# Kernel optimization log

Hardware: AMD Instinct MI355X
Metric: run time of the kernel (lower is better)

Reference implementation:

```python
import jax, jax.numpy as jnp
import numpy as np

B, N, E, DIN, DOUT = 4, 10000, 320000, 128, 128
EPS = 1e-5


def setup_inputs() -> dict:
    key = jax.random.key(0)
    ks = jax.random.split(key, 10)
    x = jax.random.normal(ks[0], (B, N, DIN), dtype=jnp.float32)
    edge_index = jax.random.randint(ks[1], (2, E), 0, N, dtype=jnp.int64)
    norm = jax.random.uniform(ks[2], (E, 1), dtype=jnp.float32)
    W_w = jax.random.normal(ks[3], (DOUT, DIN), dtype=jnp.float32) / np.sqrt(DIN)
    W_b = jax.random.normal(ks[4], (DOUT,), dtype=jnp.float32) * 0.01
    bn_gamma = jnp.ones((N,), dtype=jnp.float32)
    bn_beta = jnp.zeros((N,), dtype=jnp.float32)
    bn_mean = jax.random.normal(ks[5], (N,), dtype=jnp.float32) * 0.01
    bn_var = jax.random.uniform(ks[6], (N,), dtype=jnp.float32, minval=0.5, maxval=1.5)
    return {"x": x, "edge_index": edge_index, "norm": norm, "W_w": W_w,
            "W_b": W_b, "bn_gamma": bn_gamma, "bn_beta": bn_beta,
            "bn_mean": bn_mean, "bn_var": bn_var}


def reference(x, edge_index, norm, W_w, W_b, bn_gamma, bn_beta, bn_mean, bn_var):
    # Dropout is identity in eval mode.
    h = jnp.einsum('bnf,of->bno', x, W_w) + W_b            # [B, N, DOUT]
    # BatchNorm1d over channel dim = node dim (eval mode, running stats)
    inv = jax.lax.rsqrt(bn_var + EPS)
    h = (h - bn_mean[None, :, None]) * (inv * bn_gamma)[None, :, None] + bn_beta[None, :, None]
    h = jax.nn.gelu(h, approximate=False)                  # torch GELU default = exact erf
    # gather -> scale -> scatter-add message passing
    msgs = h[:, edge_index[1], :] * norm                   # [B, E, DOUT]
    out = jnp.zeros_like(h).at[:, edge_index[0], :].add(msgs)
    return out
```

## Files before the change

kernel.cpp:

```cpp
#include <hip/hip_runtime.h>
#include <math.h>

#define DIN 128
#define DOUT 128
#define EPS 1e-5f
#define CAP 128

typedef unsigned short ushort_t;
typedef __bf16 bf16x8 __attribute__((ext_vector_type(8)));
typedef float f32x16 __attribute__((ext_vector_type(16)));

__device__ __forceinline__ unsigned int f2bf_u(float f) {
    union { float f; unsigned int i; } v; v.f = f;
    unsigned int x = v.i;
    unsigned int r = x + 0x7fffu + ((x >> 16) & 1u);
    return r >> 16;
}
__device__ __forceinline__ ushort_t f2bf(float f) { return (ushort_t)f2bf_u(f); }

__global__ __launch_bounds__(256) void prep_kernel(
    const float* __restrict__ W, uint4* __restrict__ wb,
    int* __restrict__ counts, int N)
{
    int t = blockIdx.x * blockDim.x + threadIdx.x;
    if (t < 2048) {
        int ct = t >> 9, kc = (t >> 6) & 7, l = t & 63;
        int o = ct * 32 + (l & 31);
        int f = kc * 16 + ((l >> 5) << 3);
        const float4* src = (const float4*)(W + o * 128 + f);
        float4 v0 = src[0], v1 = src[1];
        uint4 pk;
        pk.x = f2bf_u(v0.x) | (f2bf_u(v0.y) << 16);
        pk.y = f2bf_u(v0.z) | (f2bf_u(v0.w) << 16);
        pk.z = f2bf_u(v1.x) | (f2bf_u(v1.y) << 16);
        pk.w = f2bf_u(v1.z) | (f2bf_u(v1.w) << 16);
        wb[t] = pk;
    }
    for (int i = t; i < N; i += gridDim.x * blockDim.x) counts[i] = 0;
}

__global__ __launch_bounds__(256, 4) void gemm_bn_gelu_fill(
    const float* __restrict__ x, const uint4* __restrict__ wb,
    const float* __restrict__ bias, const float* __restrict__ gamma,
    const float* __restrict__ beta, const float* __restrict__ mean,
    const float* __restrict__ var, ushort_t* __restrict__ hb,
    const int* __restrict__ ei, const float* __restrict__ norm,
    int* __restrict__ counts, unsigned int* __restrict__ csr,
    int N, int E)
{
    __shared__ ushort_t XH[8192];
    __shared__ float sm_mu[16], sm_sc[16], sm_bt[16];

    const int tid = threadIdx.x;
    const int n0 = blockIdx.x * 16;
    const int w = tid >> 6;
    const int lane = tid & 63;

    bf16x8 bfr[8];
#pragma unroll
    for (int kc = 0; kc < 8; ++kc)
        bfr[kc] = *(const bf16x8*)(wb + (w * 512 + kc * 64 + lane));

    {
        const int gid = blockIdx.x * blockDim.x + tid;
        const int stride = gridDim.x * blockDim.x;
        for (int e = gid; e < E; e += 2 * stride) {
            int ep = e + stride;
            int has2 = ep < E;
            int dst0 = ei[e];
            int src0 = ei[E + e];
            float nm0 = norm[e];
            int dst1 = 0, src1 = 0;
            float nm1 = 0.f;
            if (has2) { dst1 = ei[ep]; src1 = ei[E + ep]; nm1 = norm[ep]; }
            int slot0 = atomicAdd(&counts[dst0], 1);
            if (slot0 < CAP)
                csr[(size_t)dst0 * CAP + slot0] =
                    ((unsigned int)src0 << 16) | f2bf_u(nm0);
            if (has2) {
                int slot1 = atomicAdd(&counts[dst1], 1);
                if (slot1 < CAP)
                    csr[(size_t)dst1 * CAP + slot1] =
                        ((unsigned int)src1 << 16) | f2bf_u(nm1);
            }
        }
    }

    if (tid < 16) {
        int n = n0 + tid;
        sm_mu[tid] = mean[n];
        sm_sc[tid] = rsqrtf(var[n] + EPS) * gamma[n];
        sm_bt[tid] = beta[n];
    }

#pragma unroll
    for (int it = 0; it < 4; ++it) {
        int tup = tid + it * 256;
        int rt = tup >> 9, kc = (tup >> 6) & 7, l = tup & 63;
        int r = rt * 32 + (l & 31);
        int b = r >> 4, i = r & 15;
        size_t grow = (size_t)b * N + n0 + i;
        int f = kc * 16 + ((l >> 5) << 3);
        const float4* src = (const float4*)(x + grow * 128 + f);
        float4 v0 = src[0], v1 = src[1];
        uint4 pk;
        pk.x = f2bf_u(v0.x) | (f2bf_u(v0.y) << 16);
        pk.y = f2bf_u(v0.z) | (f2bf_u(v0.w) << 16);
        pk.z = f2bf_u(v1.x) | (f2bf_u(v1.y) << 16);
        pk.w = f2bf_u(v1.z) | (f2bf_u(v1.w) << 16);
        *(uint4*)&XH[tup * 8] = pk;
    }
    __syncthreads();

    f32x16 acc0 = {};
    f32x16 acc1 = {};
#pragma unroll
    for (int kc = 0; kc < 8; ++kc) {
        bf16x8 a0 = *(const bf16x8*)&XH[(kc * 64 + lane) * 8];
        bf16x8 a1 = *(const bf16x8*)&XH[(512 * 8) + (kc * 64 + lane) * 8];
        acc0 = __builtin_amdgcn_mfma_f32_32x32x16_bf16(a0, bfr[kc], acc0, 0, 0, 0);
        acc1 = __builtin_amdgcn_mfma_f32_32x32x16_bf16(a1, bfr[kc], acc1, 0, 0, 0);
    }
    __syncthreads();

    const int col = w * 32 + (lane & 31);
    const float bias_c = bias[col];
    const int hi4 = (lane >> 5) * 4;
#pragma unroll
    for (int reg = 0; reg < 8; ++reg) {
        int i0 = (reg & 3) + 8 * (reg >> 2) + hi4;
        float mu = sm_mu[i0], sc = sm_sc[i0], bt = sm_bt[i0];
        float vals[4] = { acc0[reg], acc0[reg + 8], acc1[reg], acc1[reg + 8] };
        ushort4 pk;
        {
            float v = vals[0] + bias_c; v = (v - mu) * sc + bt;
            pk.x = f2bf(0.5f * v * (1.0f + erff(v * 0.70710678118654752f)));
        }
        {
            float v = vals[1] + bias_c; v = (v - mu) * sc + bt;
            pk.y = f2bf(0.5f * v * (1.0f + erff(v * 0.70710678118654752f)));
        }
        {
            float v = vals[2] + bias_c; v = (v - mu) * sc + bt;
            pk.z = f2bf(0.5f * v * (1.0f + erff(v * 0.70710678118654752f)));
        }
        {
            float v = vals[3] + bias_c; v = (v - mu) * sc + bt;
            pk.w = f2bf(0.5f * v * (1.0f + erff(v * 0.70710678118654752f)));
        }
        *(ushort4*)&XH[((i0 << 7) + col) << 2] = pk;
    }
    __syncthreads();

    {
        const float4* s = (const float4*)XH;
        float4* d = (float4*)(hb + (size_t)n0 * 512);
#pragma unroll
        for (int i = tid; i < 1024; i += 256) d[i] = s[i];
    }
}

__device__ __forceinline__ void fma8(float* acc, int4 h, float wgt) {
    union { unsigned int i; float f; } t;
    unsigned int u;
    u = (unsigned int)h.x;
    t.i = u << 16;          acc[0] = fmaf(t.f, wgt, acc[0]);
    t.i = u & 0xffff0000u;  acc[1] = fmaf(t.f, wgt, acc[1]);
    u = (unsigned int)h.y;
    t.i = u << 16;          acc[2] = fmaf(t.f, wgt, acc[2]);
    t.i = u & 0xffff0000u;  acc[3] = fmaf(t.f, wgt, acc[3]);
    u = (unsigned int)h.z;
    t.i = u << 16;          acc[4] = fmaf(t.f, wgt, acc[4]);
    t.i = u & 0xffff0000u;  acc[5] = fmaf(t.f, wgt, acc[5]);
    u = (unsigned int)h.w;
    t.i = u << 16;          acc[6] = fmaf(t.f, wgt, acc[6]);
    t.i = u & 0xffff0000u;  acc[7] = fmaf(t.f, wgt, acc[7]);
}

__global__ __launch_bounds__(256) void gather_kernel(
    const ushort_t* __restrict__ hb, const int* __restrict__ counts,
    const unsigned int* __restrict__ csr, float* __restrict__ out, int N)
{
    const int w = threadIdx.x >> 6;
    const int lane = threadIdx.x & 63;
    const int n = blockIdx.x * 4 + w;
    if (n >= N) return;

    int cnt = counts[n];
    if (cnt > CAP) cnt = CAP;
    const unsigned int* bucket = csr + (size_t)n * CAP;

    float acc[8] = {};
    for (int base = 0; base < cnt; base += 64) {
        int lim = cnt - base; if (lim > 64) lim = 64;
        unsigned int meta = bucket[base + lane];
        int j = 0;
        for (; j + 8 <= lim; j += 8) {
            unsigned int m0 = (unsigned int)__builtin_amdgcn_readlane((int)meta, j);
            unsigned int m1 = (unsigned int)__builtin_amdgcn_readlane((int)meta, j + 1);
            unsigned int m2 = (unsigned int)__builtin_amdgcn_readlane((int)meta, j + 2);
            unsigned int m3 = (unsigned int)__builtin_amdgcn_readlane((int)meta, j + 3);
            unsigned int m4 = (unsigned int)__builtin_amdgcn_readlane((int)meta, j + 4);
            unsigned int m5 = (unsigned int)__builtin_amdgcn_readlane((int)meta, j + 5);
            unsigned int m6 = (unsigned int)__builtin_amdgcn_readlane((int)meta, j + 6);
            unsigned int m7 = (unsigned int)__builtin_amdgcn_readlane((int)meta, j + 7);
            int4 h0 = *(const int4*)(hb + (size_t)(m0 >> 16) * 512 + lane * 8);
            int4 h1 = *(const int4*)(hb + (size_t)(m1 >> 16) * 512 + lane * 8);
            int4 h2 = *(const int4*)(hb + (size_t)(m2 >> 16) * 512 + lane * 8);
            int4 h3 = *(const int4*)(hb + (size_t)(m3 >> 16) * 512 + lane * 8);
            int4 h4 = *(const int4*)(hb + (size_t)(m4 >> 16) * 512 + lane * 8);
            int4 h5 = *(const int4*)(hb + (size_t)(m5 >> 16) * 512 + lane * 8);
            int4 h6 = *(const int4*)(hb + (size_t)(m6 >> 16) * 512 + lane * 8);
            int4 h7 = *(const int4*)(hb + (size_t)(m7 >> 16) * 512 + lane * 8);
            union { unsigned int i; float f; } wv;
            wv.i = m0 << 16; fma8(acc, h0, wv.f);
            wv.i = m1 << 16; fma8(acc, h1, wv.f);
            wv.i = m2 << 16; fma8(acc, h2, wv.f);
            wv.i = m3 << 16; fma8(acc, h3, wv.f);
            wv.i = m4 << 16; fma8(acc, h4, wv.f);
            wv.i = m5 << 16; fma8(acc, h5, wv.f);
            wv.i = m6 << 16; fma8(acc, h6, wv.f);
            wv.i = m7 << 16; fma8(acc, h7, wv.f);
        }
        for (; j < lim; ++j) {
            unsigned int m = (unsigned int)__builtin_amdgcn_readlane((int)meta, j);
            int4 hv = *(const int4*)(hb + (size_t)(m >> 16) * 512 + lane * 8);
            union { unsigned int i; float f; } wv;
            wv.i = m << 16;
            fma8(acc, hv, wv.f);
        }
    }

    const size_t bstride = (size_t)N * DOUT;
    float* op = out + (size_t)n * DOUT + lane * 2;
#pragma unroll
    for (int b = 0; b < 4; ++b) {
        float2 v; v.x = acc[b]; v.y = acc[4 + b];
        *(float2*)(op + b * bstride) = v;
    }
}

extern "C" void kernel_launch(void* const* d_in, const int* in_sizes, int n_in,
                              void* d_out, int out_size, void* d_ws, size_t ws_size,
                              hipStream_t stream)
{
    const float* x     = (const float*)d_in[0];
    const int*   ei    = (const int*)d_in[1];
    const float* norm  = (const float*)d_in[2];
    const float* W_w   = (const float*)d_in[3];
    const float* W_b   = (const float*)d_in[4];
    const float* gamma = (const float*)d_in[5];
    const float* beta  = (const float*)d_in[6];
    const float* mean  = (const float*)d_in[7];
    const float* var   = (const float*)d_in[8];
    float* out = (float*)d_out;

    const int N = in_sizes[5];
    const int E = in_sizes[2];

    ushort_t* hb      = (ushort_t*)d_ws;
    uint4* wb         = (uint4*)(hb + (size_t)N * 512);
    int* counts       = (int*)(wb + 2048);
    unsigned int* csr = (unsigned int*)(counts + N);

    int prep_blocks = (N + 255) / 256;
    prep_kernel<<<prep_blocks, 256, 0, stream>>>(W_w, wb, counts, N);

    int gemm_blocks = N / 16;
    gemm_bn_gelu_fill<<<gemm_blocks, 256, 0, stream>>>(
        x, wb, W_b, gamma, beta, mean, var, hb, ei, norm, counts, csr, N, E);

    gather_kernel<<<(N + 3) / 4, 256, 0, stream>>>(hb, counts, csr, out, N);
}
```

Measured before the change: 152.1 us.

## Bucket CSR edges per destination by source chunk for gather locality

The per-destination edge bucket is split into sub-buckets keyed by the source-node chunk (2048 nodes), each holding up to 32 entries. The gather then walks the chunks in order, so all waves touch roughly the same region of the bf16 activation table at the same time, which should improve L2 hit rates. In exchange it adds more counters to zero, extra per-chunk loop overhead, and padded 8-wide iterations that read row 0 with zero weight. A per-chunk cap of 32 can drop edges if a chunk holds more than 32 in-edges for one node, where the old cap was 128 per node.

```diff
diff --git a/kernel.cpp b/kernel.cpp
--- a/kernel.cpp
+++ b/kernel.cpp
@@ -4,7 +4,8 @@
 #define DIN 128
 #define DOUT 128
 #define EPS 1e-5f
-#define CAP 128
+#define CHUNK_SHIFT 11
+#define CAPC 32
 
 typedef unsigned short ushort_t;
 typedef __bf16 bf16x8 __attribute__((ext_vector_type(8)));
@@ -20,7 +21,7 @@
 
 __global__ __launch_bounds__(256) void prep_kernel(
     const float* __restrict__ W, uint4* __restrict__ wb,
-    int* __restrict__ counts, int N)
+    int* __restrict__ counts, int total_counts)
 {
     int t = blockIdx.x * blockDim.x + threadIdx.x;
     if (t < 2048) {
@@ -36,7 +37,7 @@
         pk.w = f2bf_u(v1.z) | (f2bf_u(v1.w) << 16);
         wb[t] = pk;
     }
-    for (int i = t; i < N; i += gridDim.x * blockDim.x) counts[i] = 0;
+    for (int i = t; i < total_counts; i += gridDim.x * blockDim.x) counts[i] = 0;
 }
 
 __global__ __launch_bounds__(256, 4) void gemm_bn_gelu_fill(
@@ -46,7 +47,7 @@
     const float* __restrict__ var, ushort_t* __restrict__ hb,
     const int* __restrict__ ei, const float* __restrict__ norm,
     int* __restrict__ counts, unsigned int* __restrict__ csr,
-    int N, int E)
+    int N, int E, int nc)
 {
     __shared__ ushort_t XH[8192];
     __shared__ float sm_mu[16], sm_sc[16], sm_bt[16];
@@ -73,14 +74,16 @@
             int dst1 = 0, src1 = 0;
             float nm1 = 0.f;
             if (has2) { dst1 = ei[ep]; src1 = ei[E + ep]; nm1 = norm[ep]; }
-            int slot0 = atomicAdd(&counts[dst0], 1);
-            if (slot0 < CAP)
-                csr[(size_t)dst0 * CAP + slot0] =
+            int b0 = dst0 * nc + (src0 >> CHUNK_SHIFT);
+            int slot0 = atomicAdd(&counts[b0], 1);
+            if (slot0 < CAPC)
+                csr[((size_t)b0 << 5) + slot0] =
                     ((unsigned int)src0 << 16) | f2bf_u(nm0);
             if (has2) {
-                int slot1 = atomicAdd(&counts[dst1], 1);
-                if (slot1 < CAP)
-                    csr[(size_t)dst1 * CAP + slot1] =
+                int b1 = dst1 * nc + (src1 >> CHUNK_SHIFT);
+                int slot1 = atomicAdd(&counts[b1], 1);
+                if (slot1 < CAPC)
+                    csr[((size_t)b1 << 5) + slot1] =
                         ((unsigned int)src1 << 16) | f2bf_u(nm1);
             }
         }
@@ -179,55 +182,48 @@
 
 __global__ __launch_bounds__(256) void gather_kernel(
     const ushort_t* __restrict__ hb, const int* __restrict__ counts,
-    const unsigned int* __restrict__ csr, float* __restrict__ out, int N)
+    const unsigned int* __restrict__ csr, float* __restrict__ out,
+    int N, int nc)
 {
     const int w = threadIdx.x >> 6;
     const int lane = threadIdx.x & 63;
     const int n = blockIdx.x * 4 + w;
     if (n >= N) return;
 
-    int cnt = counts[n];
-    if (cnt > CAP) cnt = CAP;
-    const unsigned int* bucket = csr + (size_t)n * CAP;
-
     float acc[8] = {};
-    for (int base = 0; base < cnt; base += 64) {
-        int lim = cnt - base; if (lim > 64) lim = 64;
-        unsigned int meta = bucket[base + lane];
-        int j = 0;
-        for (; j + 8 <= lim; j += 8) {
-            unsigned int m0 = (unsigned int)__builtin_amdgcn_readlane((int)meta, j);
-            unsigned int m1 = (unsigned int)__builtin_amdgcn_readlane((int)meta, j + 1);
-            unsigned int m2 = (unsigned int)__builtin_amdgcn_readlane((int)meta, j + 2);
-            unsigned int m3 = (unsigned int)__builtin_amdgcn_readlane((int)meta, j + 3);
-            unsigned int m4 = (unsigned int)__builtin_amdgcn_readlane((int)meta, j + 4);
-            unsigned int m5 = (unsigned int)__builtin_amdgcn_readlane((int)meta, j + 5);
-            unsigned int m6 = (unsigned int)__builtin_amdgcn_readlane((int)meta, j + 6);
-            unsigned int m7 = (unsigned int)__builtin_amdgcn_readlane((int)meta, j + 7);
-            int4 h0 = *(const int4*)(hb + (size_t)(m0 >> 16) * 512 + lane * 8);
-            int4 h1 = *(const int4*)(hb + (size_t)(m1 >> 16) * 512 + lane * 8);
-            int4 h2 = *(const int4*)(hb + (size_t)(m2 >> 16) * 512 + lane * 8);
-            int4 h3 = *(const int4*)(hb + (size_t)(m3 >> 16) * 512 + lane * 8);
-            int4 h4 = *(const int4*)(hb + (size_t)(m4 >> 16) * 512 + lane * 8);
-            int4 h5 = *(const int4*)(hb + (size_t)(m5 >> 16) * 512 + lane * 8);
-            int4 h6 = *(const int4*)(hb + (size_t)(m6 >> 16) * 512 + lane * 8);
-            int4 h7 = *(const int4*)(hb + (size_t)(m7 >> 16) * 512 + lane * 8);
+    const int l2 = lane & (CAPC - 1);
+
+    for (int c = 0; c < nc; ++c) {
+        int cnt = counts[n * nc + c];
+        if (cnt > CAPC) cnt = CAPC;
+        if (cnt == 0) continue;
+        const unsigned int* bucket = csr + ((size_t)(n * nc + c) << 5);
+        unsigned int meta = bucket[l2];
+        for (int j = 0; j < cnt; j += 8) {
+            unsigned int m[8];
+#pragma unroll
+            for (int k = 0; k < 8; ++k) {
+                unsigned int mk =
+                    (unsigned int)__builtin_amdgcn_readlane((int)meta, j + k);
+                m[k] = (j + k < cnt) ? mk : 0u;
+            }
+            int4 h0 = *(const int4*)(hb + (size_t)(m[0] >> 16) * 512 + lane * 8);
+            int4 h1 = *(const int4*)(hb + (size_t)(m[1] >> 16) * 512 + lane * 8);
+            int4 h2 = *(const int4*)(hb + (size_t)(m[2] >> 16) * 512 + lane * 8);
+            int4 h3 = *(const int4*)(hb + (size_t)(m[3] >> 16) * 512 + lane * 8);
+            int4 h4 = *(const int4*)(hb + (size_t)(m[4] >> 16) * 512 + lane * 8);
+            int4 h5 = *(const int4*)(hb + (size_t)(m[5] >> 16) * 512 + lane * 8);
+            int4 h6 = *(const int4*)(hb + (size_t)(m[6] >> 16) * 512 + lane * 8);
+            int4 h7 = *(const int4*)(hb + (size_t)(m[7] >> 16) * 512 + lane * 8);
             union { unsigned int i; float f; } wv;
-            wv.i = m0 << 16; fma8(acc, h0, wv.f);
-            wv.i = m1 << 16; fma8(acc, h1, wv.f);
-            wv.i = m2 << 16; fma8(acc, h2, wv.f);
-            wv.i = m3 << 16; fma8(acc, h3, wv.f);
-            wv.i = m4 << 16; fma8(acc, h4, wv.f);
-            wv.i = m5 << 16; fma8(acc, h5, wv.f);
-            wv.i = m6 << 16; fma8(acc, h6, wv.f);
-            wv.i = m7 << 16; fma8(acc, h7, wv.f);
-        }
-        for (; j < lim; ++j) {
-            unsigned int m = (unsigned int)__builtin_amdgcn_readlane((int)meta, j);
-            int4 hv = *(const int4*)(hb + (size_t)(m >> 16) * 512 + lane * 8);
-            union { unsigned int i; float f; } wv;
-            wv.i = m << 16;
-            fma8(acc, hv, wv.f);
+            wv.i = m[0] << 16; fma8(acc, h0, wv.f);
+            wv.i = m[1] << 16; fma8(acc, h1, wv.f);
+            wv.i = m[2] << 16; fma8(acc, h2, wv.f);
+            wv.i = m[3] << 16; fma8(acc, h3, wv.f);
+            wv.i = m[4] << 16; fma8(acc, h4, wv.f);
+            wv.i = m[5] << 16; fma8(acc, h5, wv.f);
+            wv.i = m[6] << 16; fma8(acc, h6, wv.f);
+            wv.i = m[7] << 16; fma8(acc, h7, wv.f);
         }
     }
 
@@ -257,18 +253,19 @@
 
     const int N = in_sizes[5];
     const int E = in_sizes[2];
+    const int nc = (N + (1 << CHUNK_SHIFT) - 1) >> CHUNK_SHIFT;
 
     ushort_t* hb      = (ushort_t*)d_ws;
     uint4* wb         = (uint4*)(hb + (size_t)N * 512);
     int* counts       = (int*)(wb + 2048);
-    unsigned int* csr = (unsigned int*)(counts + N);
-
-    int prep_blocks = (N + 255) / 256;
-    prep_kernel<<<prep_blocks, 256, 0, stream>>>(W_w, wb, counts, N);
+    unsigned int* csr = (unsigned int*)(counts + (size_t)N * nc);
+
+    int prep_blocks = (N * nc + 255) / 256;
+    prep_kernel<<<prep_blocks, 256, 0, stream>>>(W_w, wb, counts, N * nc);
 
     int gemm_blocks = N / 16;
     gemm_bn_gelu_fill<<<gemm_blocks, 256, 0, stream>>>(
-        x, wb, W_b, gamma, beta, mean, var, hb, ei, norm, counts, csr, N, E);
-
-    gather_kernel<<<(N + 3) / 4, 256, 0, stream>>>(hb, counts, csr, out, N);
-}
+        x, wb, W_b, gamma, beta, mean, var, hb, ei, norm, counts, csr, N, E, nc);
+
+    gather_kernel<<<(N + 3) / 4, 256, 0, stream>>>(hb, counts, csr, out, N, nc);
+}
```

Result: faster. 144.8 us (-4.8%).
